# Optimization experiments

Measured on AMD Instinct MI355X. Metric: run time of the kernel, lower is better.

The kernel has to match this reference:

```python
import jax, jax.numpy as jnp
import numpy as np

B, S, D_IN, D_H = 4, 2048, 1024, 1024

def setup_inputs() -> dict:
    key = jax.random.key(0)
    k1, k2, k3, k4 = jax.random.split(key, 4)
    x = jax.random.normal(k1, (B, S, D_IN), dtype=jnp.float32)
    # torch nn.Linear weights are [out, in]; kept in that layout
    Wq = jax.random.normal(k2, (D_H, D_IN), dtype=jnp.float32) * (1.0 / np.sqrt(D_IN))
    Wk = jax.random.normal(k3, (D_H, D_IN), dtype=jnp.float32) * (1.0 / np.sqrt(D_IN))
    Wv = jax.random.normal(k4, (D_H, D_IN), dtype=jnp.float32) * (1.0 / np.sqrt(D_IN))
    return {"x": x, "Wq": Wq, "Wk": Wk, "Wv": Wv}

def reference(x, Wq, Wk, Wv):
    # projections (Linear, no bias): x @ W.T
    q = jnp.einsum('bsd,hd->bsh', x, Wq)
    k = jnp.einsum('bsd,hd->bsh', x, Wk)
    v = jnp.einsum('bsd,hd->bsh', x, Wv)
    scores = jnp.einsum('bqh,bkh->bqk', q, k)  # [B,S,S]
    S_len = x.shape[1]
    causal = jnp.triu(jnp.ones((S_len, S_len), dtype=bool), k=1)
    scores = jnp.where(causal, -jnp.inf, scores) / jnp.sqrt(jnp.float32(k.shape[-1]))
    attn = jax.nn.softmax(scores, axis=-1)
    # dropout is identity in eval/deterministic mode
    return jnp.einsum('bqk,bkh->bqh', attn, v)
```

## Files before the change

kernel.cpp:

```cpp
#include <hip/hip_runtime.h>
#include <hip/hip_bf16.h>
#include <stdint.h>

typedef unsigned short u16;
typedef __attribute__((ext_vector_type(8))) short short8;
typedef __attribute__((ext_vector_type(4))) float f32x4;
typedef __attribute__((ext_vector_type(4))) u16 u16x4;

#define S_LEN 2048
#define D_DIM 1024
#define NBATCH 4
#define BM 128
#define BN 128
#define BK 32

enum { MODE_QKV = 0, MODE_SC = 2, MODE_PV = 3 };

__device__ inline u16 f2bf(float f) {
  uint32_t u = __float_as_uint(f);
  uint32_t r = (u + 0x7fffu + ((u >> 16) & 1u)) >> 16;
  return (u16)r;
}

__global__ __launch_bounds__(256) void cast_all(
    const float* __restrict__ x, const float* __restrict__ wq,
    const float* __restrict__ wk, const float* __restrict__ wv,
    u16* __restrict__ out) {
  const int X4 = (NBATCH * S_LEN * D_DIM) / 4;
  const int W4 = (D_DIM * D_DIM) / 4;
  const int total = X4 + 3 * W4;
  int g = blockIdx.x * blockDim.x + threadIdx.x;
  int stride = gridDim.x * blockDim.x;
  for (; g < total; g += stride) {
    const float* src;
    int si;
    if (g < X4) { src = x; si = g; }
    else if (g < X4 + W4) { src = wq; si = g - X4; }
    else if (g < X4 + 2 * W4) { src = wk; si = g - X4 - W4; }
    else { src = wv; si = g - X4 - 2 * W4; }
    f32x4 v = *reinterpret_cast<const f32x4*>(src + (long)si * 4);
    u16x4 o;
    o[0] = f2bf(v[0]); o[1] = f2bf(v[1]); o[2] = f2bf(v[2]); o[3] = f2bf(v[3]);
    *reinterpret_cast<u16x4*>(out + (long)g * 4) = o;
  }
}

template <int MODE>
__global__ __launch_bounds__(256, 2) void gemm_bt(
    const u16* __restrict__ A, const u16* __restrict__ B, void* __restrict__ C,
    int K, long strideAb, long strideBb, long strideCb, int ldc,
    float* __restrict__ aux, int nb) {
  __shared__ u16 As[2][BM * BK];
  __shared__ u16 Bs[2][BN * BK];
  __shared__ float ilds[BM];

  int br, bc, bz;
  if (MODE == MODE_SC) {
    int t;
    if (nb == NBATCH) {
      int lin = blockIdx.x;
      int xcd = lin & 7;
      bz = xcd >> 1;
      t = (xcd & 1) * 68 + (lin >> 3);
    } else {
      bz = blockIdx.z;
      t = blockIdx.x;
    }
    int r = (int)((sqrtf(8.0f * (float)t + 1.0f) - 1.0f) * 0.5f);
    while ((r + 1) * (r + 2) / 2 <= t) ++r;
    while (r * (r + 1) / 2 > t) --r;
    br = r;
    bc = t - r * (r + 1) / 2;
  } else if (MODE == MODE_PV) {
    int xr, bcl, ch;
    if (nb == NBATCH) {
      int lin = blockIdx.x;
      int xcd = lin & 7;
      bz = xcd >> 1;
      ch = xcd & 1;
      int rank = lin >> 3;
      xr = rank >> 2;
      bcl = rank & 3;
      br = (xr < 8) ? (15 - 2 * xr) : (2 * (xr - 8));
      bc = ch * 4 + bcl;
    } else {
      bz = blockIdx.z;
      xr = blockIdx.x;
      int nt = S_LEN / BM;
      br = (xr & 1) ? (xr >> 1) : (nt - 1 - (xr >> 1));
      bc = blockIdx.y;
    }
  } else {
    int lin = blockIdx.y * gridDim.x + blockIdx.x;
    int xcd = lin & 7;
    int rank = lin >> 3;
    br = xcd * 8 + (rank & 7);
    bc = rank >> 3;
    bz = 0;
  }

  const u16* Ab = A + (long)bz * strideAb;
  const u16* Bb = B + (long)bz * strideBb;

  const int rowBase = br * BM;
  const int colBase = bc * BN;
  int nkt = (MODE == MODE_PV) ? (br + 1) * (BM / BK) : (K / BK);

  const int tid = threadIdx.x;
  const int lane = tid & 63;
  const int wave = tid >> 6;
  const int wr = wave >> 1, wc = wave & 1;
  const int l15 = lane & 15;
  const int g = lane >> 4;
  const int gsw = (g ^ ((l15 >> 1) & 3)) * 8;

  if (MODE == MODE_PV) {
    int row = tid >> 1, half = tid & 1;
    const float* lp = aux + (long)bz * S_LEN * 32 + (long)(rowBase + row) * 32;
    int nslot = 2 * (br + 1);
    float s = 0.f;
    for (int k = half; k < nslot; k += 2) s += lp[k];
    s += __shfl_xor(s, 1);
    if (half == 0) ilds[row] = 1.f / s;
  }

  f32x4 acc[4][4];
#pragma unroll
  for (int i = 0; i < 4; i++)
#pragma unroll
    for (int j = 0; j < 4; j++) acc[i][j] = f32x4{0.f, 0.f, 0.f, 0.f};

  const int srow = tid >> 2;
  const int skc = ((tid & 3) ^ ((srow >> 1) & 3)) * 8;

  auto stage = [&](int buf, int kt) {
    const u16* ga = Ab + (long)(rowBase + srow) * K + kt * BK + skc;
    const u16* gb = Bb + (long)(colBase + srow) * K + kt * BK + skc;
    __builtin_amdgcn_global_load_lds(
        (const __attribute__((address_space(1))) void*)ga,
        (__attribute__((address_space(3))) void*)(&As[buf][tid * 8]), 16, 0, 0);
    __builtin_amdgcn_global_load_lds(
        (const __attribute__((address_space(1))) void*)(ga + (long)64 * K),
        (__attribute__((address_space(3))) void*)(&As[buf][64 * BK + tid * 8]), 16, 0, 0);
    __builtin_amdgcn_global_load_lds(
        (const __attribute__((address_space(1))) void*)gb,
        (__attribute__((address_space(3))) void*)(&Bs[buf][tid * 8]), 16, 0, 0);
    __builtin_amdgcn_global_load_lds(
        (const __attribute__((address_space(1))) void*)(gb + (long)64 * K),
        (__attribute__((address_space(3))) void*)(&Bs[buf][64 * BK + tid * 8]), 16, 0, 0);
  };

  stage(0, 0);
  __syncthreads();
  int cur = 0;
  for (int kt = 0; kt < nkt; ++kt) {
    if (kt + 1 < nkt) stage(cur ^ 1, kt + 1);
    short8 af[4], bf[4];
#pragma unroll
    for (int i = 0; i < 4; i++)
      af[i] = *reinterpret_cast<const short8*>(
          &As[cur][(wr * 64 + i * 16 + l15) * BK + gsw]);
#pragma unroll
    for (int j = 0; j < 4; j++)
      bf[j] = *reinterpret_cast<const short8*>(
          &Bs[cur][(wc * 64 + j * 16 + l15) * BK + gsw]);
#pragma unroll
    for (int i = 0; i < 4; i++)
#pragma unroll
      for (int j = 0; j < 4; j++)
        acc[i][j] = __builtin_amdgcn_mfma_f32_16x16x32_bf16(af[i], bf[j], acc[i][j], 0, 0, 0);
    __syncthreads();
    cur ^= 1;
  }

  const int lr = g * 4;
  const int lc = l15;

  if (MODE == MODE_QKV) {
    u16* Cb = (u16*)C;
    const long seg = (long)NBATCH * S_LEN * D_DIM;
    const int segi = colBase >> 10;
    const int hb = colBase & 1023;
    if (segi < 2) {
      u16* dst = Cb + (long)segi * seg;
#pragma unroll
      for (int i = 0; i < 4; i++) {
        int r0 = rowBase + wr * 64 + i * 16 + lr;
#pragma unroll
        for (int j = 0; j < 4; j++) {
          int c0 = hb + wc * 64 + j * 16 + lc;
#pragma unroll
          for (int q = 0; q < 4; q++) dst[(long)(r0 + q) * D_DIM + c0] = f2bf(acc[i][j][q]);
        }
      }
    } else {
      u16* dst = Cb + 2 * seg;
#pragma unroll
      for (int i = 0; i < 4; i++) {
        int m0 = rowBase + wr * 64 + i * 16 + lr;
        int b = m0 >> 11, s0 = m0 & (S_LEN - 1);
#pragma unroll
        for (int j = 0; j < 4; j++) {
          int h = hb + wc * 64 + j * 16 + lc;
          u16x4 o;
          o[0] = f2bf(acc[i][j][0]); o[1] = f2bf(acc[i][j][1]);
          o[2] = f2bf(acc[i][j][2]); o[3] = f2bf(acc[i][j][3]);
          *reinterpret_cast<u16x4*>(dst + ((long)b * D_DIM + h) * S_LEN + s0) = o;
        }
      }
    }
  } else if (MODE == MODE_SC) {
    u16* Cb = (u16*)C + (long)bz * strideCb;
    float* lp = aux + (long)bz * S_LEN * 32;
#pragma unroll
    for (int i = 0; i < 4; i++) {
      int r0 = rowBase + wr * 64 + i * 16 + lr;
#pragma unroll
      for (int q = 0; q < 4; q++) {
        int r = r0 + q;
        float rs = 0.f;
#pragma unroll
        for (int j = 0; j < 4; j++) {
          int c0 = colBase + wc * 64 + j * 16 + lc;
          float p = (c0 <= r) ? __expf(acc[i][j][q] * 0.03125f - 8.f) : 0.f;
          rs += p;
          Cb[(long)r * ldc + c0] = f2bf(p);
        }
#pragma unroll
        for (int off = 1; off < 16; off <<= 1) rs += __shfl_xor(rs, off);
        if ((lane & 15) == 0) lp[r * 32 + bc * 2 + wc] = rs;
      }
    }
  } else {
    float* Cb = (float*)C + (long)bz * strideCb;
#pragma unroll
    for (int i = 0; i < 4; i++) {
      int r0 = rowBase + wr * 64 + i * 16 + lr;
#pragma unroll
      for (int j = 0; j < 4; j++) {
        int c0 = colBase + wc * 64 + j * 16 + lc;
#pragma unroll
        for (int q = 0; q < 4; q++)
          Cb[(long)(r0 + q) * ldc + c0] = acc[i][j][q] * ilds[wr * 64 + i * 16 + lr + q];
      }
    }
  }
}

extern "C" void kernel_launch(void* const* d_in, const int* in_sizes, int n_in,
                              void* d_out, int out_size, void* d_ws, size_t ws_size,
                              hipStream_t stream) {
  const float* x = (const float*)d_in[0];
  const float* Wq = (const float*)d_in[1];
  const float* Wk = (const float*)d_in[2];
  const float* Wv = (const float*)d_in[3];
  float* out = (float*)d_out;

  const size_t SD = (size_t)S_LEN * D_DIM;
  const size_t SS = (size_t)S_LEN * S_LEN;
  const size_t DD = (size_t)D_DIM * D_DIM;

  size_t off = 0;
  char* ws = (char*)d_ws;
  auto alloc = [&](size_t bytes) -> char* {
    char* p = ws + off;
    off += (bytes + 255) & ~(size_t)255;
    return p;
  };
  u16* xb = (u16*)alloc((NBATCH * SD + 3 * DD) * 2);
  u16* Wqkvb = xb + NBATCH * SD;
  u16* QKVt = (u16*)alloc(3 * NBATCH * SD * 2);
  u16* Qb = QKVt;
  u16* Kb = QKVt + NBATCH * SD;
  u16* Vt = QKVt + 2 * NBATCH * SD;
  size_t base_off = off;
  size_t need_full = base_off + ((NBATCH * SS * 2 + 255) & ~(size_t)255) +
                     ((NBATCH * (size_t)S_LEN * 32 * 4 + 255) & ~(size_t)255);
  const int nbpar = (ws_size >= need_full) ? NBATCH : 1;
  u16* P = (u16*)alloc((size_t)nbpar * SS * 2);
  float* l_part = (float*)alloc((size_t)nbpar * S_LEN * 32 * 4);

  cast_all<<<2048, 256, 0, stream>>>(x, Wq, Wk, Wv, xb);

  dim3 gp((NBATCH * S_LEN) / BM, 3 * D_DIM / BN, 1);
  gemm_bt<MODE_QKV><<<gp, 256, 0, stream>>>(xb, Wqkvb, QKVt, D_DIM, 0, 0, 0, D_DIM,
                                            nullptr, NBATCH);

  const int ntri = (S_LEN / BM) * (S_LEN / BM + 1) / 2;
  if (nbpar == NBATCH) {
    gemm_bt<MODE_SC><<<dim3(8 * 68, 1, 1), 256, 0, stream>>>(
        Qb, Kb, P, D_DIM, (long)SD, (long)SD, (long)SS, S_LEN, l_part, NBATCH);
    gemm_bt<MODE_PV><<<dim3(8 * 64, 1, 1), 256, 0, stream>>>(
        P, Vt, out, S_LEN, (long)SS, (long)SD, (long)SD, D_DIM, l_part, NBATCH);
  } else {
    for (int b = 0; b < NBATCH; ++b) {
      gemm_bt<MODE_SC><<<dim3(ntri, 1, 1), 256, 0, stream>>>(
          Qb + b * SD, Kb + b * SD, P, D_DIM, 0, 0, 0, S_LEN, l_part, 1);
      gemm_bt<MODE_PV><<<dim3(S_LEN / BM, D_DIM / BN, 1), 256, 0, stream>>>(
          P, Vt + b * SD, out + b * SD, S_LEN, 0, 0, 0, D_DIM, l_part, 1);
    }
  }
}
```

Baseline: 150.2 us.

## Halve GEMM row tile to 64 and remap triangular and PV block schedules

Shrinks BM from 128 to 64 so each 4-wave block computes a 64x128 tile, with each wave owning a 64x32 slice. The triangular score-tile enumeration, the PV row ordering and the row-sum partial slots are reworked to match. The score kernel still skips only at 128-column granularity, so rows in a diagonal tile may do some extra masked work. The goal is more blocks for better occupancy and load balance across CUs and XCDs on the causal stages, at the cost of less operand reuse per block and more B-tile reloads.

```diff
diff --git a/kernel.cpp b/kernel.cpp
--- a/kernel.cpp
+++ b/kernel.cpp
@@ -10,7 +10,7 @@
 #define S_LEN 2048
 #define D_DIM 1024
 #define NBATCH 4
-#define BM 128
+#define BM 64
 #define BN 128
 #define BK 32
 
@@ -61,41 +61,42 @@
       int lin = blockIdx.x;
       int xcd = lin & 7;
       bz = xcd >> 1;
-      t = (xcd & 1) * 68 + (lin >> 3);
+      t = (xcd & 1) * 136 + (lin >> 3);
     } else {
       bz = blockIdx.z;
       t = blockIdx.x;
     }
-    int r = (int)((sqrtf(8.0f * (float)t + 1.0f) - 1.0f) * 0.5f);
-    while ((r + 1) * (r + 2) / 2 <= t) ++r;
-    while (r * (r + 1) / 2 > t) --r;
+    auto cum = [](int r) { int m = r >> 1; return (r & 1) ? (m + 1) * (m + 1) : m * (m + 1); };
+    int r = (int)(2.0f * sqrtf((float)t + 1.0f));
+    if (r > 31) r = 31;
+    while (r < 31 && cum(r + 1) <= t) ++r;
+    while (r > 0 && cum(r) > t) --r;
     br = r;
-    bc = t - r * (r + 1) / 2;
+    bc = t - cum(r);
   } else if (MODE == MODE_PV) {
-    int xr, bcl, ch;
     if (nb == NBATCH) {
       int lin = blockIdx.x;
       int xcd = lin & 7;
       bz = xcd >> 1;
-      ch = xcd & 1;
+      int ch = xcd & 1;
       int rank = lin >> 3;
-      xr = rank >> 2;
-      bcl = rank & 3;
-      br = (xr < 8) ? (15 - 2 * xr) : (2 * (xr - 8));
+      int bcl = rank & 3;
+      int xr = rank >> 2;
+      int m = xr & 7, k = xr >> 3;
+      br = (k == 0) ? 2 * m : (k == 1) ? 2 * m + 1 : (k == 2) ? 30 - 2 * m : 31 - 2 * m;
       bc = ch * 4 + bcl;
     } else {
       bz = blockIdx.z;
-      xr = blockIdx.x;
-      int nt = S_LEN / BM;
-      br = (xr & 1) ? (xr >> 1) : (nt - 1 - (xr >> 1));
+      int xr = blockIdx.x;
+      br = (xr & 1) ? (xr >> 1) : (31 - (xr >> 1));
       bc = blockIdx.y;
     }
   } else {
     int lin = blockIdx.y * gridDim.x + blockIdx.x;
     int xcd = lin & 7;
     int rank = lin >> 3;
-    br = xcd * 8 + (rank & 7);
-    bc = rank >> 3;
+    br = xcd * 16 + (rank & 15);
+    bc = rank >> 4;
     bz = 0;
   }
 
@@ -104,31 +105,31 @@
 
   const int rowBase = br * BM;
   const int colBase = bc * BN;
-  int nkt = (MODE == MODE_PV) ? (br + 1) * (BM / BK) : (K / BK);
+  int nkt = (MODE == MODE_PV) ? 4 * ((br >> 1) + 1) : (K / BK);
 
   const int tid = threadIdx.x;
   const int lane = tid & 63;
-  const int wave = tid >> 6;
-  const int wr = wave >> 1, wc = wave & 1;
+  const int wc = tid >> 6;
   const int l15 = lane & 15;
   const int g = lane >> 4;
   const int gsw = (g ^ ((l15 >> 1) & 3)) * 8;
 
   if (MODE == MODE_PV) {
-    int row = tid >> 1, half = tid & 1;
-    const float* lp = aux + (long)bz * S_LEN * 32 + (long)(rowBase + row) * 32;
-    int nslot = 2 * (br + 1);
+    int row = tid >> 2, q4 = tid & 3;
+    const float* lp = aux + (long)bz * S_LEN * 64 + (long)(rowBase + row) * 64;
+    int nslot = 4 * ((br >> 1) + 1);
     float s = 0.f;
-    for (int k = half; k < nslot; k += 2) s += lp[k];
+    for (int k = q4; k < nslot; k += 4) s += lp[k];
     s += __shfl_xor(s, 1);
-    if (half == 0) ilds[row] = 1.f / s;
-  }
-
-  f32x4 acc[4][4];
+    s += __shfl_xor(s, 2);
+    if (q4 == 0) ilds[row] = 1.f / s;
+  }
+
+  f32x4 acc[4][2];
 #pragma unroll
   for (int i = 0; i < 4; i++)
 #pragma unroll
-    for (int j = 0; j < 4; j++) acc[i][j] = f32x4{0.f, 0.f, 0.f, 0.f};
+    for (int j = 0; j < 2; j++) acc[i][j] = f32x4{0.f, 0.f, 0.f, 0.f};
 
   const int srow = tid >> 2;
   const int skc = ((tid & 3) ^ ((srow >> 1) & 3)) * 8;
@@ -140,9 +141,6 @@
         (const __attribute__((address_space(1))) void*)ga,
         (__attribute__((address_space(3))) void*)(&As[buf][tid * 8]), 16, 0, 0);
     __builtin_amdgcn_global_load_lds(
-        (const __attribute__((address_space(1))) void*)(ga + (long)64 * K),
-        (__attribute__((address_space(3))) void*)(&As[buf][64 * BK + tid * 8]), 16, 0, 0);
-    __builtin_amdgcn_global_load_lds(
         (const __attribute__((address_space(1))) void*)gb,
         (__attribute__((address_space(3))) void*)(&Bs[buf][tid * 8]), 16, 0, 0);
     __builtin_amdgcn_global_load_lds(
@@ -155,19 +153,19 @@
   int cur = 0;
   for (int kt = 0; kt < nkt; ++kt) {
     if (kt + 1 < nkt) stage(cur ^ 1, kt + 1);
-    short8 af[4], bf[4];
+    short8 af[4], bf[2];
 #pragma unroll
     for (int i = 0; i < 4; i++)
       af[i] = *reinterpret_cast<const short8*>(
-          &As[cur][(wr * 64 + i * 16 + l15) * BK + gsw]);
-#pragma unroll
-    for (int j = 0; j < 4; j++)
+          &As[cur][(i * 16 + l15) * BK + gsw]);
+#pragma unroll
+    for (int j = 0; j < 2; j++)
       bf[j] = *reinterpret_cast<const short8*>(
-          &Bs[cur][(wc * 64 + j * 16 + l15) * BK + gsw]);
+          &Bs[cur][(wc * 32 + j * 16 + l15) * BK + gsw]);
 #pragma unroll
     for (int i = 0; i < 4; i++)
 #pragma unroll
-      for (int j = 0; j < 4; j++)
+      for (int j = 0; j < 2; j++)
         acc[i][j] = __builtin_amdgcn_mfma_f32_16x16x32_bf16(af[i], bf[j], acc[i][j], 0, 0, 0);
     __syncthreads();
     cur ^= 1;
@@ -185,10 +183,10 @@
       u16* dst = Cb + (long)segi * seg;
 #pragma unroll
       for (int i = 0; i < 4; i++) {
-        int r0 = rowBase + wr * 64 + i * 16 + lr;
-#pragma unroll
-        for (int j = 0; j < 4; j++) {
-          int c0 = hb + wc * 64 + j * 16 + lc;
+        int r0 = rowBase + i * 16 + lr;
+#pragma unroll
+        for (int j = 0; j < 2; j++) {
+          int c0 = hb + wc * 32 + j * 16 + lc;
 #pragma unroll
           for (int q = 0; q < 4; q++) dst[(long)(r0 + q) * D_DIM + c0] = f2bf(acc[i][j][q]);
         }
@@ -197,11 +195,11 @@
       u16* dst = Cb + 2 * seg;
 #pragma unroll
       for (int i = 0; i < 4; i++) {
-        int m0 = rowBase + wr * 64 + i * 16 + lr;
+        int m0 = rowBase + i * 16 + lr;
         int b = m0 >> 11, s0 = m0 & (S_LEN - 1);
 #pragma unroll
-        for (int j = 0; j < 4; j++) {
-          int h = hb + wc * 64 + j * 16 + lc;
+        for (int j = 0; j < 2; j++) {
+          int h = hb + wc * 32 + j * 16 + lc;
           u16x4 o;
           o[0] = f2bf(acc[i][j][0]); o[1] = f2bf(acc[i][j][1]);
           o[2] = f2bf(acc[i][j][2]); o[3] = f2bf(acc[i][j][3]);
@@ -211,37 +209,37 @@
     }
   } else if (MODE == MODE_SC) {
     u16* Cb = (u16*)C + (long)bz * strideCb;
-    float* lp = aux + (long)bz * S_LEN * 32;
+    float* lp = aux + (long)bz * S_LEN * 64;
 #pragma unroll
     for (int i = 0; i < 4; i++) {
-      int r0 = rowBase + wr * 64 + i * 16 + lr;
+      int r0 = rowBase + i * 16 + lr;
 #pragma unroll
       for (int q = 0; q < 4; q++) {
         int r = r0 + q;
         float rs = 0.f;
 #pragma unroll
-        for (int j = 0; j < 4; j++) {
-          int c0 = colBase + wc * 64 + j * 16 + lc;
+        for (int j = 0; j < 2; j++) {
+          int c0 = colBase + wc * 32 + j * 16 + lc;
           float p = (c0 <= r) ? __expf(acc[i][j][q] * 0.03125f - 8.f) : 0.f;
           rs += p;
           Cb[(long)r * ldc + c0] = f2bf(p);
         }
 #pragma unroll
         for (int off = 1; off < 16; off <<= 1) rs += __shfl_xor(rs, off);
-        if ((lane & 15) == 0) lp[r * 32 + bc * 2 + wc] = rs;
+        if ((lane & 15) == 0) lp[r * 64 + bc * 4 + wc] = rs;
       }
     }
   } else {
     float* Cb = (float*)C + (long)bz * strideCb;
 #pragma unroll
     for (int i = 0; i < 4; i++) {
-      int r0 = rowBase + wr * 64 + i * 16 + lr;
-#pragma unroll
-      for (int j = 0; j < 4; j++) {
-        int c0 = colBase + wc * 64 + j * 16 + lc;
+      int rl0 = i * 16 + lr;
+#pragma unroll
+      for (int j = 0; j < 2; j++) {
+        int c0 = colBase + wc * 32 + j * 16 + lc;
 #pragma unroll
         for (int q = 0; q < 4; q++)
-          Cb[(long)(r0 + q) * ldc + c0] = acc[i][j][q] * ilds[wr * 64 + i * 16 + lr + q];
+          Cb[(long)(rowBase + rl0 + q) * ldc + c0] = acc[i][j][q] * ilds[rl0 + q];
       }
     }
   }
@@ -275,10 +273,10 @@
   u16* Vt = QKVt + 2 * NBATCH * SD;
   size_t base_off = off;
   size_t need_full = base_off + ((NBATCH * SS * 2 + 255) & ~(size_t)255) +
-                     ((NBATCH * (size_t)S_LEN * 32 * 4 + 255) & ~(size_t)255);
+                     ((NBATCH * (size_t)S_LEN * 64 * 4 + 255) & ~(size_t)255);
   const int nbpar = (ws_size >= need_full) ? NBATCH : 1;
   u16* P = (u16*)alloc((size_t)nbpar * SS * 2);
-  float* l_part = (float*)alloc((size_t)nbpar * S_LEN * 32 * 4);
+  float* l_part = (float*)alloc((size_t)nbpar * S_LEN * 64 * 4);
 
   cast_all<<<2048, 256, 0, stream>>>(x, Wq, Wk, Wv, xb);
 
@@ -286,17 +284,16 @@
   gemm_bt<MODE_QKV><<<gp, 256, 0, stream>>>(xb, Wqkvb, QKVt, D_DIM, 0, 0, 0, D_DIM,
                                             nullptr, NBATCH);
 
-  const int ntri = (S_LEN / BM) * (S_LEN / BM + 1) / 2;
   if (nbpar == NBATCH) {
-    gemm_bt<MODE_SC><<<dim3(8 * 68, 1, 1), 256, 0, stream>>>(
+    gemm_bt<MODE_SC><<<dim3(8 * 136, 1, 1), 256, 0, stream>>>(
         Qb, Kb, P, D_DIM, (long)SD, (long)SD, (long)SS, S_LEN, l_part, NBATCH);
-    gemm_bt<MODE_PV><<<dim3(8 * 64, 1, 1), 256, 0, stream>>>(
+    gemm_bt<MODE_PV><<<dim3(8 * 128, 1, 1), 256, 0, stream>>>(
         P, Vt, out, S_LEN, (long)SS, (long)SD, (long)SD, D_DIM, l_part, NBATCH);
   } else {
     for (int b = 0; b < NBATCH; ++b) {
-      gemm_bt<MODE_SC><<<dim3(ntri, 1, 1), 256, 0, stream>>>(
+      gemm_bt<MODE_SC><<<dim3(272, 1, 1), 256, 0, stream>>>(
           Qb + b * SD, Kb + b * SD, P, D_DIM, 0, 0, 0, S_LEN, l_part, 1);
-      gemm_bt<MODE_PV><<<dim3(S_LEN / BM, D_DIM / BN, 1), 256, 0, stream>>>(
+      gemm_bt<MODE_PV><<<dim3(32, 8, 1), 256, 0, stream>>>(
           P, Vt + b * SD, out + b * SD, S_LEN, 0, 0, 0, D_DIM, l_part, 1);
     }
   }
```

Result: slower. 167.5 us (+11.5%).
